# Kernel optimization log

Measured on AMD Instinct MI355X. Metric: run time of the kernel, lower is better.

Reference implementation:

```python
import jax, jax.numpy as jnp
import numpy as np
from functools import partial

THRESH = 0.6      # objectness sigmoid threshold (forward arg `thresh`)
CASE = 416.0      # input image size (forward arg `case`)
NMS_THRESH = 0.7  # nms(boxes, 0.7, mode='inter')
K_PER_SCALE = 512 # fixed candidate cap per scale (jit-safe stand-in for nonzero())
NEG = -1e9


def _decode_scale(out, t, anchors):
    """out: [N, 3*(5+nc), H, W] -> (boxes [K,9], valid [K]) top-K by objectness."""
    N, C, H, W = out.shape
    v = out.transpose(0, 2, 3, 1).reshape(N, H, W, 3, -1)  # [N,H,W,3,5+nc]
    f = v.dtype
    obj = jax.nn.sigmoid(v[..., 0])                        # cfd = sigmoid(vecs[:,0])
    gy = jnp.arange(H, dtype=f).reshape(1, H, 1, 1)        # idxs[:,1] (row)
    gx = jnp.arange(W, dtype=f).reshape(1, 1, W, 1)        # idxs[:,2] (col)
    gn = jnp.arange(N, dtype=f).reshape(N, 1, 1, 1)
    cx = (gx + v[..., 1]) * t / CASE
    cy = (gy + v[..., 2]) * t / CASE
    w = anchors[:, 0] * jnp.exp(v[..., 3]) / CASE          # anchors[a,0], a = last axis
    h = anchors[:, 1] * jnp.exp(v[..., 4]) / CASE
    cls = jnp.argmax(v[..., 5:], axis=-1).astype(f)
    parts = jnp.broadcast_arrays(gn, cx, cy, w, h, obj, cls, gy + 0 * cx, gx + 0 * cx)
    boxes = jnp.stack(parts, axis=-1).reshape(-1, 9)       # [N*H*W*3, 9]
    mask = (obj > THRESH).reshape(-1)
    score = jnp.where(mask, obj.reshape(-1), NEG)
    k = min(K_PER_SCALE, score.shape[0])
    top_s, top_i = jax.lax.top_k(score, k)
    boxes_k = jnp.take(boxes, top_i, axis=0)
    valid_k = top_s > NEG / 2
    if k < K_PER_SCALE:  # pad to fixed K
        pad = K_PER_SCALE - k
        boxes_k = jnp.concatenate([boxes_k, jnp.zeros((pad, 9), f)], 0)
        valid_k = jnp.concatenate([valid_k, jnp.zeros((pad,), bool)], 0)
    return boxes_k, valid_k


def _nms_inter(boxes, valid):
    """Greedy NMS, iou mode 'inter' = inter_area / min(area_i, area_j)."""
    score = jnp.where(valid, boxes[:, 5], NEG)
    order = jnp.argsort(-score)
    boxes = jnp.take(boxes, order, axis=0)
    valid = jnp.take(valid, order)
    cx, cy, w, h = boxes[:, 1], boxes[:, 2], boxes[:, 3], boxes[:, 4]
    x1, y1, x2, y2 = cx - w / 2, cy - h / 2, cx + w / 2, cy + h / 2
    area = jnp.maximum(x2 - x1, 0) * jnp.maximum(y2 - y1, 0)
    ix = jnp.maximum(0.0, jnp.minimum(x2[:, None], x2[None]) - jnp.maximum(x1[:, None], x1[None]))
    iy = jnp.maximum(0.0, jnp.minimum(y2[:, None], y2[None]) - jnp.maximum(y1[:, None], y1[None]))
    inter = ix * iy
    iou = inter / jnp.maximum(jnp.minimum(area[:, None], area[None]), 1e-9)
    M = boxes.shape[0]
    idx = jnp.arange(M)

    def body(i, keep):
        sup = (iou[i] > NMS_THRESH) & keep[i] & (idx > i)
        return keep & ~sup

    keep = jax.lax.fori_loop(0, M, body, valid)
    return boxes * keep[:, None].astype(boxes.dtype)  # suppressed rows zeroed


def reference(out13, out26, out52, anchors13, anchors26, anchors52):
    b13, v13 = _decode_scale(out13, 32.0, anchors13)
    b26, v26 = _decode_scale(out26, 16.0, anchors26)
    b52, v52 = _decode_scale(out52, 8.0, anchors52)
    boxes = jnp.concatenate([b13, b26, b52], axis=0)   # [3K, 9]
    valid = jnp.concatenate([v13, v26, v52], axis=0)
    return _nms_inter(boxes, valid)


def setup_inputs() -> dict:
    key = jax.random.key(0)
    k = jax.random.split(key, 6)
    N, NC = 32, 80
    C = 3 * (5 + NC)
    return {
        "out13": jax.random.normal(k[0], (N, C, 13, 13), jnp.float32),
        "out26": jax.random.normal(k[1], (N, C, 26, 26), jnp.float32),
        "out52": jax.random.normal(k[2], (N, C, 52, 52), jnp.float32),
        "anchors13": jnp.array([[116, 90], [156, 198], [373, 326]], jnp.float32),
        "anchors26": jnp.array([[30, 61], [62, 45], [59, 119]], jnp.float32),
        "anchors52": jnp.array([[10, 13], [16, 30], [33, 23]], jnp.float32),
    }
```

## Files before the change

### kernel.cpp

```cpp
#include <hip/hip_runtime.h>
#include <stdint.h>

#define KPS 512
#define NBOX 1536
#define NBINS 1024
#define CAP 96

#define S13 16224
#define S26 64896
#define S52 259584
#define TOTCELL 340704

__device__ __forceinline__ uint32_t f2u(float x){ union{float f;uint32_t u;}v; v.f=x; return v.u; }
__device__ __forceinline__ float u2f(uint32_t x){ union{float f;uint32_t u;}v; v.u=x; return v.f; }

__device__ __forceinline__ int binOf(float s){
    int b = (int)((s - 0.6f) * 2560.0f);
    if (b < 0) b = 0;
    if (b > NBINS-1) b = NBINS-1;
    return b;
}

__device__ __forceinline__ unsigned long long readlane64(unsigned long long v, int i){
    unsigned lo = (unsigned)__builtin_amdgcn_readlane((int)(unsigned)v, i);
    unsigned hi = (unsigned)__builtin_amdgcn_readlane((int)(unsigned)(v >> 32), i);
    return ((unsigned long long)hi << 32) | (unsigned long long)lo;
}

__global__ void k_init(int* hist, int* cnt){
    int id = blockIdx.x*256 + threadIdx.x;
    if (id < 3*NBINS) hist[id] = 0;
    if (id < 32) cnt[id] = 0;
}

__global__ void k_score(const float* __restrict__ o13, const float* __restrict__ o26,
                        const float* __restrict__ o52,
                        unsigned long long* __restrict__ bucket, int* __restrict__ hist){
    int id = blockIdx.x*256 + threadIdx.x;
    if (id >= TOTCELL) return;
    int scale, idl, H;
    const float* src;
    if (id < S13)            { scale=0; idl=id;            H=13; src=o13; }
    else if (id < S13+S26)   { scale=1; idl=id-S13;        H=26; src=o26; }
    else                     { scale=2; idl=id-(S13+S26);  H=52; src=o52; }
    int HW = H*H;
    int p  = idl / HW;
    int hw = idl - p*HW;
    int n  = p / 3;
    int a  = p - n*3;
    float x = src[(size_t)(n*255 + a*85)*HW + hw];
    float s = (float)(1.0 / (1.0 + exp(-(double)x)));
    if (s > 0.6f){
        int cidx = (n*HW + hw)*3 + a;
        unsigned long long key = ((unsigned long long)f2u(s) << 20)
            | ((unsigned long long)(2-scale) << 18)
            | (unsigned long long)(262143 - cidx);
        int slot = scale*NBINS + binOf(s);
        int pos = atomicAdd(&hist[slot], 1);
        if (pos < CAP) bucket[(size_t)slot*CAP + pos] = key;
    }
}

__global__ void __launch_bounds__(1024) k_selfin(const int* __restrict__ hist,
                        const unsigned long long* __restrict__ bucket,
                        unsigned long long* __restrict__ sel, int* __restrict__ cnt){
    int s = blockIdx.x, t = threadIdx.x;
    __shared__ int suf[NBINS];
    __shared__ unsigned long long un[640];
    __shared__ int sB;
    int h = hist[s*NBINS + t];
    suf[t] = h; __syncthreads();
    for (int d = 1; d < NBINS; d <<= 1){
        int v = (t + d < NBINS) ? suf[t + d] : 0;
        __syncthreads();
        suf[t] += v;
        __syncthreads();
    }
    int total = suf[0];
    int A = (t < NBINS-1) ? suf[t+1] : 0;
    if (t == 0 && total < KPS) sB = -1;
    if (A < KPS && A + h >= KPS) sB = t;
    __syncthreads();
    int B = sB;
    int Bg = (B < 0) ? 0 : B;
    if (t + Bg < NBINS){
        int b = Bg + t;
        int cb = hist[s*NBINS + b]; if (cb > CAP) cb = CAP;
        int off = (b == NBINS-1) ? 0 : suf[b+1];
        for (int e = 0; e < cb; e++)
            un[off + e] = bucket[(size_t)(s*NBINS + b)*CAP + e];
    }
    __syncthreads();
    int hB = hist[s*NBINS + Bg]; if (hB > CAP) hB = CAP;
    int E = ((Bg == NBINS-1) ? 0 : suf[Bg+1]) + hB;
    int Nsel = (E < KPS) ? E : KPS;
    for (int e = t; e < E; e += 1024){
        unsigned long long k = un[e];
        int rank = 0;
        for (int q = 0; q < E; q++) rank += (un[q] > k) ? 1 : 0;
        if (rank < Nsel) sel[s*KPS + rank] = k;
    }
    if (t < KPS && t >= Nsel) sel[s*KPS + t] = 0ull;
    if (t == 0) cnt[s] = Nsel;
}

__global__ void __launch_bounds__(1024) k_decode_merge(
                         const float* __restrict__ o13, const float* __restrict__ o26,
                         const float* __restrict__ o52,
                         const float* __restrict__ a13, const float* __restrict__ a26,
                         const float* __restrict__ a52,
                         const unsigned long long* __restrict__ sel, const int* __restrict__ cnt,
                         float* __restrict__ sboxes, unsigned long long* __restrict__ vwords){
    __shared__ unsigned long long sk[NBOX];
    int t = threadIdx.x;
    for (int r = t; r < NBOX; r += 1024) sk[r] = sel[r];
    __syncthreads();
    int wv = t >> 6, lane = t & 63;
    int b = blockIdx.x*16 + wv;
    unsigned long long key = sk[b];
    int pc = 0;
    for (int q = lane; q < NBOX; q += 64){
        unsigned long long kq = sk[q];
        pc += (kq > key || (kq == key && q < b)) ? 1 : 0;
    }
    #pragma unroll
    for (int off = 32; off; off >>= 1) pc += __shfl_xor(pc, off);
    int rank = pc;
    float* row = sboxes + rank*12;
    if ((key >> 20) == 0ull){
        if (lane < 9) row[lane] = 0.f;
    } else {
        int scale = 2 - (int)((key >> 18) & 3ull);
        int cidx  = 262143 - (int)(key & 0x3FFFFull);
        uint32_t sbits = (uint32_t)(key >> 20);
        const float* src; const float* anch; int H; float tt;
        if (scale == 0){ src=o13; anch=a13; H=13; tt=32.f; }
        else if (scale == 1){ src=o26; anch=a26; H=26; tt=16.f; }
        else { src=o52; anch=a52; H=52; tt=8.f; }
        int HW = H*H;
        int a  = cidx % 3;
        int hw = (cidx/3) % HW;
        int n  = cidx / (3*HW);
        int hh = hw / H;
        int ww = hw - hh*H;
        const float* cellbase = src + (size_t)(n*255 + a*85)*HW + hw;
        float bv = cellbase[(size_t)(5 + lane)*HW];
        int bi = lane;
        if (lane < 16){
            float v2 = cellbase[(size_t)(69 + lane)*HW];
            if (v2 > bv){ bv = v2; bi = 64 + lane; }
        }
        #pragma unroll
        for (int off=32; off; off>>=1){
            float vo = __shfl_xor(bv, off);
            int io = __shfl_xor(bi, off);
            if (vo > bv || (vo == bv && io < bi)){ bv = vo; bi = io; }
        }
        if (lane == 0){
            float v1 = cellbase[(size_t)1*HW];
            float v2 = cellbase[(size_t)2*HW];
            float v3 = cellbase[(size_t)3*HW];
            float v4 = cellbase[(size_t)4*HW];
            float cx = ((float)ww + v1) * tt / 416.0f;
            float cy = ((float)hh + v2) * tt / 416.0f;
            float e3 = (float)exp((double)v3);
            float e4 = (float)exp((double)v4);
            float bw = anch[a*2+0] * e3 / 416.0f;
            float bh = anch[a*2+1] * e4 / 416.0f;
            row[0] = (float)n;  row[1] = cx; row[2] = cy; row[3] = bw; row[4] = bh;
            row[5] = u2f(sbits); row[6] = (float)bi; row[7] = (float)hh; row[8] = (float)ww;
        }
    }
    if (blockIdx.x == 0 && t < 24){
        int nv = cnt[0] + cnt[1] + cnt[2];
        int rem = nv - t*64;
        vwords[t] = rem >= 64 ? ~0ull : (rem <= 0 ? 0ull : ((1ull << rem) - 1ull));
    }
}

__global__ void k_masks(const float* __restrict__ sboxes, unsigned* __restrict__ Tcol,
                        unsigned long long* __restrict__ diagR){
    int i = blockIdx.x;
    int lane = threadIdx.x;
    int gi = i >> 6;
    float cxi = sboxes[i*12+1], cyi = sboxes[i*12+2], wi = sboxes[i*12+3], hi = sboxes[i*12+4];
    float x1i = cxi - wi/2.0f, y1i = cyi - hi/2.0f, x2i = cxi + wi/2.0f, y2i = cyi + hi/2.0f;
    float ari = fmaxf(x2i-x1i, 0.f) * fmaxf(y2i-y1i, 0.f);
    unsigned colbits = 0u;
    for (int c=0; c<24; c++){
        int j = c*64 + lane;
        float cxj = sboxes[j*12+1], cyj = sboxes[j*12+2], wj = sboxes[j*12+3], hj = sboxes[j*12+4];
        float x1j = cxj - wj/2.0f, y1j = cyj - hj/2.0f, x2j = cxj + wj/2.0f, y2j = cyj + hj/2.0f;
        float arj = fmaxf(x2j-x1j, 0.f) * fmaxf(y2j-y1j, 0.f);
        float ix = fmaxf(0.f, fminf(x2i, x2j) - fmaxf(x1i, x1j));
        float iy = fmaxf(0.f, fminf(y2i, y2j) - fmaxf(y1i, y1j));
        float inter = ix * iy;
        float iou = inter / fmaxf(fminf(ari, arj), 1e-9f);
        bool sb = (iou > 0.7f) && (j > i);
        colbits |= sb ? (1u << c) : 0u;
    }
    Tcol[(size_t)i*64 + lane] = colbits;
    unsigned long long rowbits = __ballot(((colbits >> gi) & 1u) != 0u);
    if (lane == 0) diagR[i] = rowbits;
}

__global__ void k_nms_out(const float* __restrict__ sboxes, const unsigned long long* __restrict__ vwords,
                          const unsigned long long* __restrict__ diagR, const unsigned* __restrict__ Tcol,
                          float* __restrict__ out){
    __shared__ unsigned long long keepw[24];
    __shared__ unsigned partial[2][4][64];
    int t = threadIdx.x;
    int wv = t >> 6, lane = t & 63;
    unsigned SS = 0u;
    unsigned long long rowR = diagR[lane];
    unsigned long long vcur = vwords[0];
    unsigned rows[16];
    {
        const unsigned* b0 = Tcol + (size_t)(wv*16)*64 + lane;
        #pragma unroll
        for (int i=0;i<16;i++) rows[i] = b0[i*64];
    }
    for (int g = 0; g < 24; g++){
        unsigned long long Rnext = (g < 23) ? diagR[(g+1)*64 + lane] : 0ull;
        unsigned long long vnext = (g < 23) ? vwords[g+1] : 0ull;
        bool live = (((vcur >> lane) & 1ull) != 0ull) && (((SS >> g) & 1u) == 0u);
        unsigned long long pend = __ballot(live);
        unsigned long long Z = __ballot(live && ((rowR & pend) != 0ull));
        unsigned long long kept = pend;
        unsigned long long iter = Z;
        while (iter){
            int i = __ffsll((long long)iter) - 1;
            iter &= iter - 1ull;
            if ((kept >> i) & 1ull){
                unsigned long long sup = readlane64(rowR, i);
                kept &= ~sup;
                iter &= ~sup;
            }
        }
        if (t == 0) keepw[g] = kept;
        unsigned kbits = (unsigned)((kept >> (wv*16)) & 0xFFFFull);
        unsigned acc = 0u;
        #pragma unroll
        for (int i=0;i<16;i++) acc |= (0u - ((kbits >> i) & 1u)) & rows[i];
        if (g < 23){
            const unsigned* nb = Tcol + (size_t)((g+1)*64 + wv*16)*64 + lane;
            #pragma unroll
            for (int i=0;i<16;i++) rows[i] = nb[i*64];
        }
        partial[g & 1][wv][lane] = acc;
        __syncthreads();
        SS |= partial[g & 1][0][lane] | partial[g & 1][1][lane]
            | partial[g & 1][2][lane] | partial[g & 1][3][lane];
        rowR = Rnext; vcur = vnext;
    }
    for (int e=t; e<NBOX*9; e+=256){
        int r = e / 9;
        int c = e - r*9;
        bool kp = ((keepw[r >> 6] >> (r & 63)) & 1ull) != 0ull;
        out[e] = kp ? sboxes[r*12 + c] : 0.f;
    }
}

extern "C" void kernel_launch(void* const* d_in, const int* in_sizes, int n_in,
                              void* d_out, int out_size, void* d_ws, size_t ws_size,
                              hipStream_t stream){
    const float* o13 = (const float*)d_in[0];
    const float* o26 = (const float*)d_in[1];
    const float* o52 = (const float*)d_in[2];
    const float* a13 = (const float*)d_in[3];
    const float* a26 = (const float*)d_in[4];
    const float* a52 = (const float*)d_in[5];
    char* ws = (char*)d_ws;
    unsigned long long* bucket = (unsigned long long*)(ws);
    unsigned* Tcol            = (unsigned*)(ws);
    int* hist                 = (int*)(ws + 2359296);
    int* cnt                  = (int*)(ws + 2371584);
    unsigned long long* sel   = (unsigned long long*)(ws + 2371712);
    float* sboxes             = (float*)(ws + 2384000);
    unsigned long long* vw    = (unsigned long long*)(ws + 2457728);
    unsigned long long* diagR = (unsigned long long*)(ws + 2457984);
    float* out = (float*)d_out;

    k_init        <<<12, 256, 0, stream>>>(hist, cnt);
    k_score       <<<(TOTCELL + 255)/256, 256, 0, stream>>>(o13, o26, o52, bucket, hist);
    k_selfin      <<<3, 1024, 0, stream>>>(hist, bucket, sel, cnt);
    k_decode_merge<<<96, 1024, 0, stream>>>(o13, o26, o52, a13, a26, a52, sel, cnt, sboxes, vw);
    k_masks       <<<NBOX, 64, 0, stream>>>(sboxes, Tcol, diagR);
    k_nms_out     <<<1, 256, 0, stream>>>(sboxes, vw, diagR, Tcol, out);
}
```

Before: 230.7 us.

## Fuse decode and IoU mask kernels, recomputing box geometry per block in LDS

Merges the decode/merge kernel and the mask kernel into one launch of 192 blocks. The first 96 blocks do the ranked decode as before. The other 96 each recompute every box's rank and geometry into shared memory, then build the suppression bitmasks from LDS instead of reading sboxes from global memory. This removes one launch and the dependency between the two kernels. In exchange, every mask block repeats an O(N^2) rank scan and the box loads.

```diff
diff --git a/kernel.cpp b/kernel.cpp
--- a/kernel.cpp
+++ b/kernel.cpp
@@ -104,104 +104,153 @@
     if (t == 0) cnt[s] = Nsel;
 }
 
-__global__ void __launch_bounds__(1024) k_decode_merge(
+__global__ void __launch_bounds__(1024) k_decmask(
                          const float* __restrict__ o13, const float* __restrict__ o26,
                          const float* __restrict__ o52,
                          const float* __restrict__ a13, const float* __restrict__ a26,
                          const float* __restrict__ a52,
                          const unsigned long long* __restrict__ sel, const int* __restrict__ cnt,
-                         float* __restrict__ sboxes, unsigned long long* __restrict__ vwords){
+                         float* __restrict__ sboxes, unsigned long long* __restrict__ vwords,
+                         unsigned* __restrict__ Tcol, unsigned long long* __restrict__ diagR){
     __shared__ unsigned long long sk[NBOX];
+    __shared__ float gx[NBOX], gy[NBOX], gw[NBOX], gh[NBOX];
     int t = threadIdx.x;
+    int blk = blockIdx.x;
     for (int r = t; r < NBOX; r += 1024) sk[r] = sel[r];
     __syncthreads();
-    int wv = t >> 6, lane = t & 63;
-    int b = blockIdx.x*16 + wv;
-    unsigned long long key = sk[b];
-    int pc = 0;
-    for (int q = lane; q < NBOX; q += 64){
-        unsigned long long kq = sk[q];
-        pc += (kq > key || (kq == key && q < b)) ? 1 : 0;
-    }
-    #pragma unroll
-    for (int off = 32; off; off >>= 1) pc += __shfl_xor(pc, off);
-    int rank = pc;
-    float* row = sboxes + rank*12;
-    if ((key >> 20) == 0ull){
-        if (lane < 9) row[lane] = 0.f;
+    if (blk < 96){
+        int wv = t >> 6, lane = t & 63;
+        int b = blk*16 + wv;
+        unsigned long long key = sk[b];
+        int pc = 0;
+        for (int q = lane; q < NBOX; q += 64){
+            unsigned long long kq = sk[q];
+            pc += (kq > key || (kq == key && q < b)) ? 1 : 0;
+        }
+        #pragma unroll
+        for (int off = 32; off; off >>= 1) pc += __shfl_xor(pc, off);
+        int rank = pc;
+        float* row = sboxes + rank*12;
+        if ((key >> 20) == 0ull){
+            if (lane < 9) row[lane] = 0.f;
+        } else {
+            int scale = 2 - (int)((key >> 18) & 3ull);
+            int cidx  = 262143 - (int)(key & 0x3FFFFull);
+            uint32_t sbits = (uint32_t)(key >> 20);
+            const float* src; const float* anch; int H; float tt;
+            if (scale == 0){ src=o13; anch=a13; H=13; tt=32.f; }
+            else if (scale == 1){ src=o26; anch=a26; H=26; tt=16.f; }
+            else { src=o52; anch=a52; H=52; tt=8.f; }
+            int HW = H*H;
+            int a  = cidx % 3;
+            int hw = (cidx/3) % HW;
+            int n  = cidx / (3*HW);
+            int hh = hw / H;
+            int ww = hw - hh*H;
+            const float* cellbase = src + (size_t)(n*255 + a*85)*HW + hw;
+            float bv = cellbase[(size_t)(5 + lane)*HW];
+            int bi = lane;
+            if (lane < 16){
+                float v2 = cellbase[(size_t)(69 + lane)*HW];
+                if (v2 > bv){ bv = v2; bi = 64 + lane; }
+            }
+            #pragma unroll
+            for (int off=32; off; off>>=1){
+                float vo = __shfl_xor(bv, off);
+                int io = __shfl_xor(bi, off);
+                if (vo > bv || (vo == bv && io < bi)){ bv = vo; bi = io; }
+            }
+            if (lane == 0){
+                float v1 = cellbase[(size_t)1*HW];
+                float v2 = cellbase[(size_t)2*HW];
+                float v3 = cellbase[(size_t)3*HW];
+                float v4 = cellbase[(size_t)4*HW];
+                float cx = ((float)ww + v1) * tt / 416.0f;
+                float cy = ((float)hh + v2) * tt / 416.0f;
+                float e3 = (float)exp((double)v3);
+                float e4 = (float)exp((double)v4);
+                float bw = anch[a*2+0] * e3 / 416.0f;
+                float bh = anch[a*2+1] * e4 / 416.0f;
+                row[0] = (float)n;  row[1] = cx; row[2] = cy; row[3] = bw; row[4] = bh;
+                row[5] = u2f(sbits); row[6] = (float)bi; row[7] = (float)hh; row[8] = (float)ww;
+            }
+        }
+        if (blk == 0 && t < 24){
+            int nv = cnt[0] + cnt[1] + cnt[2];
+            int rem = nv - t*64;
+            vwords[t] = rem >= 64 ? ~0ull : (rem <= 0 ? 0ull : ((1ull << rem) - 1ull));
+        }
     } else {
-        int scale = 2 - (int)((key >> 18) & 3ull);
-        int cidx  = 262143 - (int)(key & 0x3FFFFull);
-        uint32_t sbits = (uint32_t)(key >> 20);
-        const float* src; const float* anch; int H; float tt;
-        if (scale == 0){ src=o13; anch=a13; H=13; tt=32.f; }
-        else if (scale == 1){ src=o26; anch=a26; H=26; tt=16.f; }
-        else { src=o52; anch=a52; H=52; tt=8.f; }
-        int HW = H*H;
-        int a  = cidx % 3;
-        int hw = (cidx/3) % HW;
-        int n  = cidx / (3*HW);
-        int hh = hw / H;
-        int ww = hw - hh*H;
-        const float* cellbase = src + (size_t)(n*255 + a*85)*HW + hw;
-        float bv = cellbase[(size_t)(5 + lane)*HW];
-        int bi = lane;
-        if (lane < 16){
-            float v2 = cellbase[(size_t)(69 + lane)*HW];
-            if (v2 > bv){ bv = v2; bi = 64 + lane; }
+        int b1 = t, b2 = t + 1024;
+        unsigned long long k1 = sk[b1];
+        unsigned long long k2 = (b2 < NBOX) ? sk[b2] : 0ull;
+        int r1 = 0, r2 = 0;
+        #pragma unroll 4
+        for (int q = 0; q < NBOX; q++){
+            unsigned long long kq = sk[q];
+            r1 += (kq > k1 || (kq == k1 && q < b1)) ? 1 : 0;
+            if (b2 < NBOX) r2 += (kq > k2 || (kq == k2 && q < b2)) ? 1 : 0;
         }
         #pragma unroll
-        for (int off=32; off; off>>=1){
-            float vo = __shfl_xor(bv, off);
-            int io = __shfl_xor(bi, off);
-            if (vo > bv || (vo == bv && io < bi)){ bv = vo; bi = io; }
-        }
-        if (lane == 0){
-            float v1 = cellbase[(size_t)1*HW];
-            float v2 = cellbase[(size_t)2*HW];
-            float v3 = cellbase[(size_t)3*HW];
-            float v4 = cellbase[(size_t)4*HW];
-            float cx = ((float)ww + v1) * tt / 416.0f;
-            float cy = ((float)hh + v2) * tt / 416.0f;
-            float e3 = (float)exp((double)v3);
-            float e4 = (float)exp((double)v4);
-            float bw = anch[a*2+0] * e3 / 416.0f;
-            float bh = anch[a*2+1] * e4 / 416.0f;
-            row[0] = (float)n;  row[1] = cx; row[2] = cy; row[3] = bw; row[4] = bh;
-            row[5] = u2f(sbits); row[6] = (float)bi; row[7] = (float)hh; row[8] = (float)ww;
-        }
-    }
-    if (blockIdx.x == 0 && t < 24){
-        int nv = cnt[0] + cnt[1] + cnt[2];
-        int rem = nv - t*64;
-        vwords[t] = rem >= 64 ? ~0ull : (rem <= 0 ? 0ull : ((1ull << rem) - 1ull));
-    }
-}
-
-__global__ void k_masks(const float* __restrict__ sboxes, unsigned* __restrict__ Tcol,
-                        unsigned long long* __restrict__ diagR){
-    int i = blockIdx.x;
-    int lane = threadIdx.x;
-    int gi = i >> 6;
-    float cxi = sboxes[i*12+1], cyi = sboxes[i*12+2], wi = sboxes[i*12+3], hi = sboxes[i*12+4];
-    float x1i = cxi - wi/2.0f, y1i = cyi - hi/2.0f, x2i = cxi + wi/2.0f, y2i = cyi + hi/2.0f;
-    float ari = fmaxf(x2i-x1i, 0.f) * fmaxf(y2i-y1i, 0.f);
-    unsigned colbits = 0u;
-    for (int c=0; c<24; c++){
-        int j = c*64 + lane;
-        float cxj = sboxes[j*12+1], cyj = sboxes[j*12+2], wj = sboxes[j*12+3], hj = sboxes[j*12+4];
-        float x1j = cxj - wj/2.0f, y1j = cyj - hj/2.0f, x2j = cxj + wj/2.0f, y2j = cyj + hj/2.0f;
-        float arj = fmaxf(x2j-x1j, 0.f) * fmaxf(y2j-y1j, 0.f);
-        float ix = fmaxf(0.f, fminf(x2i, x2j) - fmaxf(x1i, x1j));
-        float iy = fmaxf(0.f, fminf(y2i, y2j) - fmaxf(y1i, y1j));
-        float inter = ix * iy;
-        float iou = inter / fmaxf(fminf(ari, arj), 1e-9f);
-        bool sb = (iou > 0.7f) && (j > i);
-        colbits |= sb ? (1u << c) : 0u;
-    }
-    Tcol[(size_t)i*64 + lane] = colbits;
-    unsigned long long rowbits = __ballot(((colbits >> gi) & 1u) != 0u);
-    if (lane == 0) diagR[i] = rowbits;
+        for (int pass = 0; pass < 2; pass++){
+            int b = pass ? b2 : b1;
+            if (b >= NBOX) continue;
+            unsigned long long key = pass ? k2 : k1;
+            int rank = pass ? r2 : r1;
+            float cx = 0.f, cy = 0.f, bw = 0.f, bh = 0.f;
+            if ((key >> 20) != 0ull){
+                int scale = 2 - (int)((key >> 18) & 3ull);
+                int cidx  = 262143 - (int)(key & 0x3FFFFull);
+                const float* src; const float* anch; int H; float tt;
+                if (scale == 0){ src=o13; anch=a13; H=13; tt=32.f; }
+                else if (scale == 1){ src=o26; anch=a26; H=26; tt=16.f; }
+                else { src=o52; anch=a52; H=52; tt=8.f; }
+                int HW = H*H;
+                int a  = cidx % 3;
+                int hw = (cidx/3) % HW;
+                int n  = cidx / (3*HW);
+                int hh = hw / H;
+                int ww = hw - hh*H;
+                const float* cellbase = src + (size_t)(n*255 + a*85)*HW + hw;
+                float v1 = cellbase[(size_t)1*HW];
+                float v2 = cellbase[(size_t)2*HW];
+                float v3 = cellbase[(size_t)3*HW];
+                float v4 = cellbase[(size_t)4*HW];
+                cx = ((float)ww + v1) * tt / 416.0f;
+                cy = ((float)hh + v2) * tt / 416.0f;
+                float e3 = (float)exp((double)v3);
+                float e4 = (float)exp((double)v4);
+                bw = anch[a*2+0] * e3 / 416.0f;
+                bh = anch[a*2+1] * e4 / 416.0f;
+            }
+            gx[rank] = cx; gy[rank] = cy; gw[rank] = bw; gh[rank] = bh;
+        }
+        __syncthreads();
+        int wv = t >> 6, lane = t & 63;
+        int i = (blk - 96)*16 + wv;
+        int gi = i >> 6;
+        float cxi = gx[i], cyi = gy[i], wi = gw[i], hi = gh[i];
+        float x1i = cxi - wi/2.0f, y1i = cyi - hi/2.0f, x2i = cxi + wi/2.0f, y2i = cyi + hi/2.0f;
+        float ari = fmaxf(x2i-x1i, 0.f) * fmaxf(y2i-y1i, 0.f);
+        unsigned colbits = 0u;
+        unsigned long long dm = 0ull;
+        for (int c=0; c<24; c++){
+            int j = c*64 + lane;
+            float cxj = gx[j], cyj = gy[j], wj = gw[j], hj = gh[j];
+            float x1j = cxj - wj/2.0f, y1j = cyj - hj/2.0f, x2j = cxj + wj/2.0f, y2j = cyj + hj/2.0f;
+            float arj = fmaxf(x2j-x1j, 0.f) * fmaxf(y2j-y1j, 0.f);
+            float ix = fmaxf(0.f, fminf(x2i, x2j) - fmaxf(x1i, x1j));
+            float iy = fmaxf(0.f, fminf(y2i, y2j) - fmaxf(y1i, y1j));
+            float inter = ix * iy;
+            float iou = inter / fmaxf(fminf(ari, arj), 1e-9f);
+            bool sb = (iou > 0.7f) && (j > i);
+            colbits |= sb ? (1u << c) : 0u;
+            unsigned long long m = __ballot(sb);
+            if (c == gi) dm = m;
+        }
+        Tcol[(size_t)i*64 + lane] = colbits;
+        if (lane == 0) diagR[i] = dm;
+    }
 }
 
 __global__ void k_nms_out(const float* __restrict__ sboxes, const unsigned long long* __restrict__ vwords,
@@ -281,10 +330,9 @@
     unsigned long long* diagR = (unsigned long long*)(ws + 2457984);
     float* out = (float*)d_out;
 
-    k_init        <<<12, 256, 0, stream>>>(hist, cnt);
-    k_score       <<<(TOTCELL + 255)/256, 256, 0, stream>>>(o13, o26, o52, bucket, hist);
-    k_selfin      <<<3, 1024, 0, stream>>>(hist, bucket, sel, cnt);
-    k_decode_merge<<<96, 1024, 0, stream>>>(o13, o26, o52, a13, a26, a52, sel, cnt, sboxes, vw);
-    k_masks       <<<NBOX, 64, 0, stream>>>(sboxes, Tcol, diagR);
-    k_nms_out     <<<1, 256, 0, stream>>>(sboxes, vw, diagR, Tcol, out);
-}
+    k_init     <<<12, 256, 0, stream>>>(hist, cnt);
+    k_score    <<<(TOTCELL + 255)/256, 256, 0, stream>>>(o13, o26, o52, bucket, hist);
+    k_selfin   <<<3, 1024, 0, stream>>>(hist, bucket, sel, cnt);
+    k_decmask  <<<192, 1024, 0, stream>>>(o13, o26, o52, a13, a26, a52, sel, cnt, sboxes, vw, Tcol, diagR);
+    k_nms_out  <<<1, 256, 0, stream>>>(sboxes, vw, diagR, Tcol, out);
+}
```

Measured after the change: 355.3 us. 54.0% more time.
